# Kernel tuning notes

Hardware: AMD Instinct MI355X
Metric: run time of the kernel (lower is better)

Reference implementation:

```python
import jax, jax.numpy as jnp
import numpy as np

B, S, E, H = 2, 4096, 768, 12
D = E // H  # head_dim = 64
SCALE = D ** -0.5
NEG = -1e9


def setup_inputs() -> dict:
    key = jax.random.key(0)
    ks = jax.random.split(key, 10)
    init = lambda k, shape: jax.random.normal(k, shape, dtype=jnp.float32) * (shape[-1] ** -0.5)
    x = jax.random.normal(ks[0], (B, S, E), dtype=jnp.float32)
    attention_mask = jnp.zeros((B, 1, S, S), dtype=jnp.float32)
    # additive causal mask: 0 on/below diagonal, -1e9 above
    causal = jnp.where(jnp.tril(jnp.ones((S, S), dtype=bool)), 0.0, NEG).astype(jnp.float32)
    causal_attention_mask = causal[None, None]
    return {
        "x": x,
        "attention_mask": attention_mask,
        "causal_attention_mask": causal_attention_mask,
        "Wq": init(ks[1], (E, E)), "bq": jnp.zeros((E,), jnp.float32),
        "Wk": init(ks[2], (E, E)), "bk": jnp.zeros((E,), jnp.float32),
        "Wv": init(ks[3], (E, E)), "bv": jnp.zeros((E,), jnp.float32),
        "Wo": init(ks[4], (E, E)), "bo": jnp.zeros((E,), jnp.float32),
    }


def _split_heads(t):
    # [B,S,E] -> [B,H,S,D]
    return t.reshape(B, S, H, D).transpose(0, 2, 1, 3)


def reference(x, attention_mask, causal_attention_mask, Wq, bq, Wk, bk, Wv, bv, Wo, bo):
    q = _split_heads(x @ Wq.T + bq)
    k = _split_heads(x @ Wk.T + bk)
    v = _split_heads(x @ Wv.T + bv)
    mask = attention_mask + causal_attention_mask  # [B,1,S,S]
    scores = jnp.einsum("bhqd,bhkd->bhqk", q, k) * SCALE + mask
    probs = jax.nn.softmax(scores.astype(jnp.float32), axis=-1).astype(q.dtype)
    out = jnp.einsum("bhqk,bhkd->bhqd", probs, v)
    out = out.transpose(0, 2, 1, 3).reshape(B, S, E)
    return out @ Wo.T + bo
```

## Files before the change

kernel.cpp:

```cpp
#include <hip/hip_runtime.h>
#include <hip/hip_bf16.h>
#include <stdint.h>

#define B_ 2
#define S_ 4096
#define E_ 768
#define H_ 12
#define D_ 64
#define M_TOT (B_*S_)
#define NQKV (3*E_)

typedef __attribute__((ext_vector_type(8)))  short bf16x8;
typedef __attribute__((ext_vector_type(4)))  float f32x4;
typedef __attribute__((ext_vector_type(16))) float f32x16;
typedef unsigned short u16;
typedef unsigned int   u32;

__device__ __forceinline__ u16 f2bf(float f) {
  __hip_bfloat16 h = __float2bfloat16(f);
  return *reinterpret_cast<u16*>(&h);
}

__device__ __forceinline__ float bf2f(u16 u) {
  union { u32 i; float f; } v; v.i = ((u32)u) << 16; return v.f;
}

__device__ __forceinline__ u32 cvtpk(float lo, float hi) {
  u32 r;
  asm("v_cvt_pk_bf16_f32 %0, %1, %2" : "=v"(r) : "v"(lo), "v"(hi));
  return r;
}

#define GLDS(gp, lp) __builtin_amdgcn_global_load_lds( \
    (const __attribute__((address_space(1))) void*)(gp), \
    (__attribute__((address_space(3))) void*)(lp), 16, 0, 0)

#define QSCALE 0.1803368801111573f


__global__ void k_cast_x(const float* __restrict__ x, u16* __restrict__ xb) {
  int i = blockIdx.x * blockDim.x + threadIdx.x;
  float4 v = reinterpret_cast<const float4*>(x)[i];
  ushort4 o;
  o.x = f2bf(v.x); o.y = f2bf(v.y); o.z = f2bf(v.z); o.w = f2bf(v.w);
  reinterpret_cast<ushort4*>(xb)[i] = o;
}

__global__ void k_pack_wqkv(const float* __restrict__ Wq, const float* __restrict__ Wk,
                            const float* __restrict__ Wv, const float* __restrict__ bq,
                            const float* __restrict__ bk, const float* __restrict__ bv,
                            u16* __restrict__ wqkv, float* __restrict__ bqkv) {
  int i = blockIdx.x * blockDim.x + threadIdx.x;
  int base = i * 4;
  int n = base / E_;
  int k = base % E_;
  const float* src; float sc;
  if (n < E_)        { src = Wq + (size_t)n*E_ + k;        sc = QSCALE; }
  else if (n < 2*E_) { src = Wk + (size_t)(n-E_)*E_ + k;   sc = 1.f; }
  else               { src = Wv + (size_t)(n-2*E_)*E_ + k; sc = 1.f; }
  float4 v = *reinterpret_cast<const float4*>(src);
  ushort4 o;
  o.x = f2bf(v.x*sc); o.y = f2bf(v.y*sc); o.z = f2bf(v.z*sc); o.w = f2bf(v.w*sc);
  reinterpret_cast<ushort4*>(wqkv)[i] = o;
  if (i < NQKV) {
    float b = (i < E_) ? bq[i]*QSCALE : (i < 2*E_) ? bk[i-E_] : bv[i-2*E_];
    bqkv[i] = b;
  }
}

__global__ void k_cast_wo(const float* __restrict__ Wo, u16* __restrict__ wo) {
  int i = blockIdx.x * blockDim.x + threadIdx.x;
  float4 v = reinterpret_cast<const float4*>(Wo)[i];
  ushort4 o;
  o.x = f2bf(v.x); o.y = f2bf(v.y); o.z = f2bf(v.z); o.w = f2bf(v.w);
  reinterpret_cast<ushort4*>(wo)[i] = o;
}


template<int MODE>
__global__ __launch_bounds__(256)
void k_gemm(const u16* __restrict__ A, const u16* __restrict__ W,
            const float* __restrict__ bias,
            u16* __restrict__ dq, u16* __restrict__ dk, u16* __restrict__ dv,
            float* __restrict__ fout)
{
  constexpr int BN = (MODE == 0) ? 128 : 64;
  constexpr int NF = BN / 32;
  __shared__ u16 As[128*64];
  __shared__ u16 Ws[BN*64];
  const int tid  = threadIdx.x;
  const int lane = tid & 63, wave = tid >> 6;
  const int m0 = blockIdx.x * 128;
  const int n0 = blockIdx.y * BN;
  const int g  = lane >> 4, cc = lane & 15;
  const int wr = (wave >> 1) * 64, wc = (wave & 1) * (BN/2);
  const int srow = lane >> 3;
  const int scol = (lane & 7) * 8;

  f32x4 acc[4][NF];
  #pragma unroll
  for (int m = 0; m < 4; ++m)
    #pragma unroll
    for (int n = 0; n < NF; ++n) acc[m][n] = (f32x4){0.f,0.f,0.f,0.f};

  for (int k0 = 0; k0 < E_; k0 += 64) {
    __syncthreads();
    #pragma unroll
    for (int i = 0; i < 4; ++i) {
      const int r0 = (i*4 + wave) * 8;
      GLDS(A + (size_t)(m0 + r0 + srow)*E_ + k0 + scol, As + r0*64);
    }
    #pragma unroll
    for (int i = 0; i < BN/32; ++i) {
      const int r0 = (i*4 + wave) * 8;
      GLDS(W + (size_t)(n0 + r0 + srow)*E_ + k0 + scol, Ws + r0*64);
    }
    __syncthreads();
    #pragma unroll
    for (int kk = 0; kk < 64; kk += 32) {
      bf16x8 af[4], bfr[NF];
      #pragma unroll
      for (int m = 0; m < 4; ++m)
        af[m] = *reinterpret_cast<const bf16x8*>(As + (wr + m*16 + cc)*64 + kk + g*8);
      #pragma unroll
      for (int n = 0; n < NF; ++n)
        bfr[n] = *reinterpret_cast<const bf16x8*>(Ws + (wc + n*16 + cc)*64 + kk + g*8);
      #pragma unroll
      for (int m = 0; m < 4; ++m)
        #pragma unroll
        for (int n = 0; n < NF; ++n)
          acc[m][n] = __builtin_amdgcn_mfma_f32_16x16x32_bf16(af[m], bfr[n], acc[m][n], 0, 0, 0);
    }
  }

  #pragma unroll
  for (int n = 0; n < NF; ++n) {
    const int colg = n0 + wc + n*16 + cc;
    const float bb = bias[colg];
    if (MODE == 0) {
      const int which = colg / E_;
      const int nn = colg % E_;
      const int h = nn >> 6, d = nn & 63;
      #pragma unroll
      for (int m = 0; m < 4; ++m)
        #pragma unroll
        for (int j = 0; j < 4; ++j) {
          const int row = m0 + wr + m*16 + g*4 + j;
          const int b = row >> 12, s = row & (S_-1);
          const u16 val = f2bf(acc[m][n][j] + bb);
          if (which == 0)       dq[(((size_t)b*H_ + h)*S_ + s)*D_ + d] = val;
          else if (which == 1)  dk[(((size_t)b*H_ + h)*S_ + s)*D_ + d] = val;
          else                  dv[(((size_t)b*H_ + h)*D_ + d)*S_ + s] = val;
        }
    } else {
      #pragma unroll
      for (int m = 0; m < 4; ++m)
        #pragma unroll
        for (int j = 0; j < 4; ++j) {
          const int row = m0 + wr + m*16 + g*4 + j;
          fout[(size_t)row*E_ + colg] = acc[m][n][j] + bb;
        }
    }
  }
}


__global__ __launch_bounds__(256, 3)
void k_attn(const u16* __restrict__ Qb, const u16* __restrict__ Kb,
            const u16* __restrict__ Vtg, u16* __restrict__ AO,
            u16* __restrict__ PO, float2* __restrict__ PML)
{
  __shared__ u16 Ks[2][32*128];
  __shared__ u16 Vs[2][32*128];
  const int tid = threadIdx.x, lane = tid & 63, w = tid >> 6;

  const int L    = blockIdx.x;
  const int slot = L >> 8;
  const int cu   = L & 255;
  const int x    = cu & 7;
  const int c    = cu >> 3;
  int r;
  if (slot < 4) r = slot*32 + ((slot & 1) ? (31 - c) : c);
  else          r = 128 + c;
  int head, qt, mode;
  if (r < 120) {
    const int g_ = r / 15, o = r % 15;
    if (o < 9) {
      if (o < 3) { head = o; qt = 15 - g_; mode = 0; }
      else { const int hh = o - 3; head = hh >> 1; mode = 1 + (hh & 1); qt = 31 - 2*g_; }
    } else { const int hh = o - 9; head = hh >> 1; mode = 1 + (hh & 1); qt = 30 - 2*g_; }
  } else {
    const int rr = r - 120; qt = 7 - rr/3; head = rr % 3; mode = 0;
  }
  const int bh = x*3 + head;
  const int q0 = qt * 128;
  const int nt = (mode == 0) ? (2*qt + 2) : (qt + 1);
  const int kvtb = (mode == 2) ? (qt + 1) : 0;

  const size_t kbase = (size_t)bh * S_ * D_;
  const size_t vbase = (size_t)bh * D_ * S_;
  const int hi = lane >> 5, l31 = lane & 31;
  const int swz = (lane & 15) << 4;
  const int qg = q0 + w*32 + l31;

  int stA[2], stB[2];
  #pragma unroll
  for (int i = 0; i < 2; ++i) {
    const int jj = 2*w + i;
    const int row = jj*4 + (lane >> 4);
    const int gb = ((lane & 15) * 16) ^ ((row & 15) << 4);
    stA[i] = row + 32*(gb >> 7);
    stB[i] = (gb & 127) >> 1;
  }

  bf16x8 qf[4];
  #pragma unroll
  for (int ds = 0; ds < 4; ++ds)
    qf[ds] = *reinterpret_cast<const bf16x8*>(Qb + kbase + (size_t)qg*D_ + ds*16 + hi*8);

  float m_run = 0.f, l_run = 0.f;
  f32x16 o0, o1, cin;
  #pragma unroll
  for (int r2 = 0; r2 < 16; ++r2) { o0[r2] = 0.f; o1[r2] = 0.f; cin[r2] = 0.f; }

#define STAGE(buf, kv0_) do { \
    _Pragma("unroll") \
    for (int i = 0; i < 2; ++i) { \
      GLDS(Kb  + kbase + (size_t)((kv0_) + stA[i])*D_ + stB[i], &Ks[buf][(2*w+i)*512]); \
      GLDS(Vtg + vbase + (size_t)stA[i]*S_ + (kv0_) + stB[i],   &Vs[buf][(2*w+i)*512]); \
    } } while(0)

  int cur = 0;
  STAGE(0, kvtb*64);

  for (int it = 0; it < nt; ++it) {
    asm volatile("s_waitcnt vmcnt(0)" ::: "memory");
    __builtin_amdgcn_s_barrier();
    asm volatile("" ::: "memory");
    if (it + 1 < nt) STAGE(cur ^ 1, (kvtb + it + 1)*64);

    const int kvt = kvtb + it;
    const int kv0 = kvt * 64;
    const u16* bK = Ks[cur];
    const u16* bV = Vs[cur];

    f32x16 s0, s1;
    __builtin_amdgcn_s_setprio(1);
    {
      const int off = (16*hi ^ swz) >> 1;
      bf16x8 a0 = *reinterpret_cast<const bf16x8*>(bK + l31*128 + off);
      bf16x8 a1 = *reinterpret_cast<const bf16x8*>(bK + l31*128 + (off ^ 64));
      s0 = __builtin_amdgcn_mfma_f32_32x32x16_bf16(a0, qf[0], cin, 0, 0, 0);
      s1 = __builtin_amdgcn_mfma_f32_32x32x16_bf16(a1, qf[0], cin, 0, 0, 0);
    }
    #pragma unroll
    for (int ds = 1; ds < 4; ++ds) {
      const int off = ((32*ds + 16*hi) ^ swz) >> 1;
      bf16x8 a0 = *reinterpret_cast<const bf16x8*>(bK + l31*128 + off);
      bf16x8 a1 = *reinterpret_cast<const bf16x8*>(bK + l31*128 + (off ^ 64));
      s0 = __builtin_amdgcn_mfma_f32_32x32x16_bf16(a0, qf[ds], s0, 0, 0, 0);
      s1 = __builtin_amdgcn_mfma_f32_32x32x16_bf16(a1, qf[ds], s1, 0, 0, 0);
    }
    __builtin_amdgcn_s_setprio(0);

    if (kvt >= 2*qt) {
      #pragma unroll
      for (int r2 = 0; r2 < 16; ++r2) {
        const int kvl = kv0 + (r2&3) + 8*(r2>>2) + 4*hi;
        s0[r2] = (kvl      > qg) ? -1e30f : s0[r2];
        s1[r2] = (kvl + 32 > qg) ? -1e30f : s1[r2];
      }
    }

    #pragma unroll
    for (int r2 = 0; r2 < 16; ++r2) s0[r2] = exp2f(s0[r2]);
    #pragma unroll
    for (int r2 = 0; r2 < 16; ++r2) s1[r2] = exp2f(s1[r2]);

    float t4[8];
    #pragma unroll
    for (int i = 0; i < 4; ++i)
      t4[i] = (s0[4*i] + s0[4*i+1]) + (s0[4*i+2] + s0[4*i+3]);
    #pragma unroll
    for (int i = 0; i < 4; ++i)
      t4[4+i] = (s1[4*i] + s1[4*i+1]) + (s1[4*i+2] + s1[4*i+3]);
    float sum = ((t4[0]+t4[1]) + (t4[2]+t4[3])) + ((t4[4]+t4[5]) + (t4[6]+t4[7]));
    sum += __shfl_xor(sum, 32);

    if (__all(sum <= 1.0995116e12f)) {
      l_run += sum;
    } else {
      const float alpha = 0x1p-40f;
      l_run = (l_run + sum) * alpha;
      m_run += 40.f;
      #pragma unroll
      for (int r2 = 0; r2 < 16; ++r2) {
        s0[r2] *= alpha; s1[r2] *= alpha;
        o0[r2] *= alpha; o1[r2] *= alpha;
        cin[r2] -= 40.f;
      }
    }

    u32 c16[16];
    #pragma unroll
    for (int i = 0; i < 8; ++i) {
      c16[i]   = cvtpk(s0[2*i], s0[2*i+1]);
      c16[8+i] = cvtpk(s1[2*i], s1[2*i+1]);
    }

    #pragma unroll
    for (int ks = 0; ks < 4; ++ks) {
      const int cb = (ks>>1)*8 + (ks&1)*4;
      u32 x0 = c16[cb],   y0 = c16[cb+2];
      u32 x1 = c16[cb+1], y1 = c16[cb+3];
      asm volatile("v_permlane32_swap_b32 %0, %1" : "+v"(x0), "+v"(y0));
      asm volatile("v_permlane32_swap_b32 %0, %1" : "+v"(x1), "+v"(y1));
      union { u32 u[4]; bf16x8 v; } pf;
      pf.u[0] = x0; pf.u[1] = x1; pf.u[2] = y0; pf.u[3] = y1;
      const int voff = ((32*ks + 16*hi) ^ swz) >> 1;
      bf16x8 v0 = *reinterpret_cast<const bf16x8*>(bV + l31*128 + voff);
      bf16x8 v1 = *reinterpret_cast<const bf16x8*>(bV + l31*128 + (voff ^ 64));
      __builtin_amdgcn_s_setprio(1);
      o0 = __builtin_amdgcn_mfma_f32_32x32x16_bf16(v0, pf.v, o0, 0, 0, 0);
      o1 = __builtin_amdgcn_mfma_f32_32x32x16_bf16(v1, pf.v, o1, 0, 0, 0);
      __builtin_amdgcn_s_setprio(0);
    }

    asm volatile("" ::: "memory");
    __builtin_amdgcn_s_barrier();
    cur ^= 1;
  }
#undef STAGE

  if (mode == 0) {
    const int b = bh / H_, h = bh % H_;
    const float inv = 1.0f / l_run;
    u16* dst = AO + ((size_t)b*S_ + qg)*E_ + h*64;
    #pragma unroll
    for (int aa = 0; aa < 4; ++aa) {
      ushort4 wv;
      wv.x = f2bf(o0[4*aa+0]*inv); wv.y = f2bf(o0[4*aa+1]*inv);
      wv.z = f2bf(o0[4*aa+2]*inv); wv.w = f2bf(o0[4*aa+3]*inv);
      *reinterpret_cast<ushort4*>(dst + aa*8 + hi*4) = wv;
    }
    #pragma unroll
    for (int aa = 0; aa < 4; ++aa) {
      ushort4 wv;
      wv.x = f2bf(o1[4*aa+0]*inv); wv.y = f2bf(o1[4*aa+1]*inv);
      wv.z = f2bf(o1[4*aa+2]*inv); wv.w = f2bf(o1[4*aa+3]*inv);
      *reinterpret_cast<ushort4*>(dst + 32 + aa*8 + hi*4) = wv;
    }
  } else {
    const int qslot = (bh*16 + (qt-16))*2 + (mode - 1);
    const int rowt = w*32 + l31;
    u16* po = PO + (size_t)qslot*(128*64) + rowt*64;
    #pragma unroll
    for (int aa = 0; aa < 4; ++aa) {
      ushort4 wv;
      wv.x = f2bf(o0[4*aa+0]); wv.y = f2bf(o0[4*aa+1]);
      wv.z = f2bf(o0[4*aa+2]); wv.w = f2bf(o0[4*aa+3]);
      *reinterpret_cast<ushort4*>(po + aa*8 + hi*4) = wv;
    }
    #pragma unroll
    for (int aa = 0; aa < 4; ++aa) {
      ushort4 wv;
      wv.x = f2bf(o1[4*aa+0]); wv.y = f2bf(o1[4*aa+1]);
      wv.z = f2bf(o1[4*aa+2]); wv.w = f2bf(o1[4*aa+3]);
      *reinterpret_cast<ushort4*>(po + 32 + aa*8 + hi*4) = wv;
    }
    if (hi == 0) PML[qslot*128 + rowt] = make_float2(m_run, l_run);
  }
}


__global__ __launch_bounds__(256)
void k_comb(const u16* __restrict__ PO, const float2* __restrict__ PML,
            u16* __restrict__ AO)
{
  const int bid = blockIdx.x;
  const int bh = bid >> 4, qi = bid & 15, q = 16 + qi;
  const int t = threadIdx.x;
  const int r = t >> 1, half = t & 1;
  const int s0 = (bh*16 + qi)*2, s1 = s0 + 1;
  const float2 ml0 = PML[s0*128 + r];
  const float2 ml1 = PML[s1*128 + r];
  const float mstar = fmaxf(ml0.x, ml1.x);
  const float w0 = exp2f(ml0.x - mstar);
  const float w1 = exp2f(ml1.x - mstar);
  const float inv = 1.0f / (ml0.y*w0 + ml1.y*w1);
  const float a0 = w0 * inv, a1 = w1 * inv;
  const u16* p0 = PO + (size_t)s0*(128*64) + r*64 + half*32;
  const u16* p1 = PO + (size_t)s1*(128*64) + r*64 + half*32;
  const int b = bh / H_, h = bh % H_;
  const int row = q*128 + r;
  u16* dst = AO + ((size_t)b*S_ + row)*E_ + h*64 + half*32;
  #pragma unroll
  for (int i = 0; i < 4; ++i) {
    bf16x8 v0 = *reinterpret_cast<const bf16x8*>(p0 + i*8);
    bf16x8 v1 = *reinterpret_cast<const bf16x8*>(p1 + i*8);
    ushort4 lo, hi4;
    float f0 = bf2f(((const u16*)&v0)[0])*a0 + bf2f(((const u16*)&v1)[0])*a1;
    float f1 = bf2f(((const u16*)&v0)[1])*a0 + bf2f(((const u16*)&v1)[1])*a1;
    float f2 = bf2f(((const u16*)&v0)[2])*a0 + bf2f(((const u16*)&v1)[2])*a1;
    float f3 = bf2f(((const u16*)&v0)[3])*a0 + bf2f(((const u16*)&v1)[3])*a1;
    lo.x = f2bf(f0); lo.y = f2bf(f1); lo.z = f2bf(f2); lo.w = f2bf(f3);
    float f4 = bf2f(((const u16*)&v0)[4])*a0 + bf2f(((const u16*)&v1)[4])*a1;
    float f5 = bf2f(((const u16*)&v0)[5])*a0 + bf2f(((const u16*)&v1)[5])*a1;
    float f6 = bf2f(((const u16*)&v0)[6])*a0 + bf2f(((const u16*)&v1)[6])*a1;
    float f7 = bf2f(((const u16*)&v0)[7])*a0 + bf2f(((const u16*)&v1)[7])*a1;
    hi4.x = f2bf(f4); hi4.y = f2bf(f5); hi4.z = f2bf(f6); hi4.w = f2bf(f7);
    *reinterpret_cast<ushort4*>(dst + i*8)     = lo;
    *reinterpret_cast<ushort4*>(dst + i*8 + 4) = hi4;
  }
}


extern "C" void kernel_launch(void* const* d_in, const int* in_sizes, int n_in,
                              void* d_out, int out_size, void* d_ws, size_t ws_size,
                              hipStream_t stream) {
  const float* x  = (const float*)d_in[0];
  const float* Wq = (const float*)d_in[3];
  const float* bq = (const float*)d_in[4];
  const float* Wk = (const float*)d_in[5];
  const float* bk = (const float*)d_in[6];
  const float* Wv = (const float*)d_in[7];
  const float* bv = (const float*)d_in[8];
  const float* Wo = (const float*)d_in[9];
  const float* bo = (const float*)d_in[10];
  float* out = (float*)d_out;

  const size_t SZ_X   = (size_t)M_TOT * E_ * 2;
  const size_t SZ_WQKV= (size_t)NQKV * E_ * 2;
  const size_t SZ_WO  = (size_t)E_ * E_ * 2;
  const size_t SZ_B   = (size_t)NQKV * 4;
  char* w = (char*)d_ws;
  u16*   xb   = (u16*)(w);
  u16*   wqkv = (u16*)(w + SZ_X);
  u16*   wob  = (u16*)(w + SZ_X + SZ_WQKV);
  float* bqkv = (float*)(w + SZ_X + SZ_WQKV + SZ_WO);
  char*  w2   = w + SZ_X + SZ_WQKV + SZ_WO + SZ_B;
  u16* Qb = (u16*)(w2);
  u16* Kb = (u16*)(w2 + SZ_X);
  u16* Vb = (u16*)(w2 + 2*SZ_X);
  u16* AO = (u16*)(w2 + 3*SZ_X);
  u16* PO = xb;
  float2* PML = (float2*)(w2 + 4*SZ_X);

  k_cast_x  <<<6144, 256, 0, stream>>>(x, xb);
  k_pack_wqkv<<<1728, 256, 0, stream>>>(Wq, Wk, Wv, bq, bk, bv, wqkv, bqkv);
  k_cast_wo <<<576,  256, 0, stream>>>(Wo, wob);

  dim3 gq(64, 18);
  k_gemm<0><<<gq, 256, 0, stream>>>(xb, wqkv, bqkv, Qb, Kb, Vb, nullptr);

  k_attn<<<1152, 256, 0, stream>>>(Qb, Kb, Vb, AO, PO, PML);
  k_comb<<<384, 256, 0, stream>>>(PO, PML, AO);

  dim3 go(64, 12);
  k_gemm<1><<<go, 256, 0, stream>>>(AO, wob, bo, nullptr, nullptr, nullptr, out);
}
```

Baseline: 200.9 us.

## Split causal attention KV loop into fixed-size chunks with multi-way combine

Replaces the hand-tuned block-to-work mapping with a uniform scheme. Each query tile's causal KV range is split into chunks of 20 KV tiles, giving up to 4 chunks for late tiles, and the grid grows to one block per chunk. The first chunk writes its unnormalized partial directly into the output buffer. The combine kernel merges 2 to 4 partials per row using the saved max and sum statistics. The trailing per-iteration barrier is also dropped, since the barrier at the top of the next iteration already protects the double buffer. This aims for better load balance across CUs, at the cost of more partial-result traffic and a larger scratch footprint that spills past the reused x buffer.

```diff
diff --git a/kernel.cpp b/kernel.cpp
--- a/kernel.cpp
+++ b/kernel.cpp
@@ -174,29 +174,23 @@
   __shared__ u16 Vs[2][32*128];
   const int tid = threadIdx.x, lane = tid & 63, w = tid >> 6;
 
-  const int L    = blockIdx.x;
-  const int slot = L >> 8;
-  const int cu   = L & 255;
-  const int x    = cu & 7;
-  const int c    = cu >> 3;
-  int r;
-  if (slot < 4) r = slot*32 + ((slot & 1) ? (31 - c) : c);
-  else          r = 128 + c;
-  int head, qt, mode;
-  if (r < 120) {
-    const int g_ = r / 15, o = r % 15;
-    if (o < 9) {
-      if (o < 3) { head = o; qt = 15 - g_; mode = 0; }
-      else { const int hh = o - 3; head = hh >> 1; mode = 1 + (hh & 1); qt = 31 - 2*g_; }
-    } else { const int hh = o - 9; head = hh >> 1; mode = 1 + (hh & 1); qt = 30 - 2*g_; }
-  } else {
-    const int rr = r - 120; qt = 7 - rr/3; head = rr % 3; mode = 0;
-  }
+  const int L   = blockIdx.x;
+  const int x   = L & 7;
+  const int idx = L >> 3;
+  const int head = idx / 68;
+  const int j    = idx % 68;
+  int qt, ch;
+  if (j < 10)      { qt = j;              ch = 0; }
+  else if (j < 30) { qt = 10 + (j-10)/2;  ch = (j-10) % 2; }
+  else if (j < 60) { qt = 20 + (j-30)/3;  ch = (j-30) % 3; }
+  else             { qt = 30 + (j-60)/4;  ch = (j-60) % 4; }
   const int bh = x*3 + head;
+  const int nc = (qt + 10) / 10;
+  const int nt_full = 2*qt + 2;
+  const int kvtb = 20 * ch;
+  const int nt_c = min(nt_full, 20*(ch+1)) - kvtb;
+
   const int q0 = qt * 128;
-  const int nt = (mode == 0) ? (2*qt + 2) : (qt + 1);
-  const int kvtb = (mode == 2) ? (qt + 1) : 0;
-
   const size_t kbase = (size_t)bh * S_ * D_;
   const size_t vbase = (size_t)bh * D_ * S_;
   const int hi = lane >> 5, l31 = lane & 31;
@@ -233,11 +227,11 @@
   int cur = 0;
   STAGE(0, kvtb*64);
 
-  for (int it = 0; it < nt; ++it) {
+  for (int it = 0; it < nt_c; ++it) {
     asm volatile("s_waitcnt vmcnt(0)" ::: "memory");
     __builtin_amdgcn_s_barrier();
     asm volatile("" ::: "memory");
-    if (it + 1 < nt) STAGE(cur ^ 1, (kvtb + it + 1)*64);
+    if (it + 1 < nt_c) STAGE(cur ^ 1, (kvtb + it + 1)*64);
 
     const int kvt = kvtb + it;
     const int kv0 = kvt * 64;
@@ -326,14 +320,12 @@
       __builtin_amdgcn_s_setprio(0);
     }
 
-    asm volatile("" ::: "memory");
-    __builtin_amdgcn_s_barrier();
     cur ^= 1;
   }
 #undef STAGE
 
-  if (mode == 0) {
-    const int b = bh / H_, h = bh % H_;
+  const int b = bh / H_, h = bh % H_;
+  if (nc == 1) {
     const float inv = 1.0f / l_run;
     u16* dst = AO + ((size_t)b*S_ + qg)*E_ + h*64;
     #pragma unroll
@@ -346,14 +338,21 @@
     #pragma unroll
     for (int aa = 0; aa < 4; ++aa) {
       ushort4 wv;
+      wv.x = f2bf(o1[4*aa+0]); wv.y = f2bf(o1[4*aa+1]);
+      wv.z = f2bf(o1[4*aa+2]); wv.w = f2bf(o1[4*aa+3]);
       wv.x = f2bf(o1[4*aa+0]*inv); wv.y = f2bf(o1[4*aa+1]*inv);
       wv.z = f2bf(o1[4*aa+2]*inv); wv.w = f2bf(o1[4*aa+3]*inv);
       *reinterpret_cast<ushort4*>(dst + 32 + aa*8 + hi*4) = wv;
     }
   } else {
-    const int qslot = (bh*16 + (qt-16))*2 + (mode - 1);
+    int mbase, pbase;
+    if (qt < 20)      { mbase = (qt-10)*2;      pbase = qt-10; }
+    else if (qt < 30) { mbase = 20+(qt-20)*3;   pbase = 10+(qt-20)*2; }
+    else              { mbase = 50+(qt-30)*4;   pbase = 30+(qt-30)*3; }
     const int rowt = w*32 + l31;
-    u16* po = PO + (size_t)qslot*(128*64) + rowt*64;
+    u16* po;
+    if (ch == 0) po = AO + ((size_t)b*S_ + qg)*E_ + h*64;
+    else         po = PO + (size_t)(bh*36 + pbase + ch-1)*(128*64) + rowt*64;
     #pragma unroll
     for (int aa = 0; aa < 4; ++aa) {
       ushort4 wv;
@@ -368,7 +367,7 @@
       wv.z = f2bf(o1[4*aa+2]); wv.w = f2bf(o1[4*aa+3]);
       *reinterpret_cast<ushort4*>(po + 32 + aa*8 + hi*4) = wv;
     }
-    if (hi == 0) PML[qslot*128 + rowt] = make_float2(m_run, l_run);
+    if (hi == 0) PML[(bh*58 + mbase + ch)*128 + rowt] = make_float2(m_run, l_run);
   }
 }
 
@@ -378,37 +377,55 @@
             u16* __restrict__ AO)
 {
   const int bid = blockIdx.x;
-  const int bh = bid >> 4, qi = bid & 15, q = 16 + qi;
+  const int bh = bid / 22, qt = 10 + bid % 22;
+  const int nc = (qt + 10) / 10;
   const int t = threadIdx.x;
   const int r = t >> 1, half = t & 1;
-  const int s0 = (bh*16 + qi)*2, s1 = s0 + 1;
-  const float2 ml0 = PML[s0*128 + r];
-  const float2 ml1 = PML[s1*128 + r];
-  const float mstar = fmaxf(ml0.x, ml1.x);
-  const float w0 = exp2f(ml0.x - mstar);
-  const float w1 = exp2f(ml1.x - mstar);
-  const float inv = 1.0f / (ml0.y*w0 + ml1.y*w1);
-  const float a0 = w0 * inv, a1 = w1 * inv;
-  const u16* p0 = PO + (size_t)s0*(128*64) + r*64 + half*32;
-  const u16* p1 = PO + (size_t)s1*(128*64) + r*64 + half*32;
+  int mbase, pbase;
+  if (qt < 20)      { mbase = (qt-10)*2;      pbase = qt-10; }
+  else if (qt < 30) { mbase = 20+(qt-20)*3;   pbase = 10+(qt-20)*2; }
+  else              { mbase = 50+(qt-30)*4;   pbase = 30+(qt-30)*3; }
+  const int mslot = bh*58 + mbase;
+  const int pslot = bh*36 + pbase;
+
+  float m[4], l[4], wgt[4];
+  float mstar = -INFINITY;
+  for (int c = 0; c < nc; ++c) {
+    float2 ml = PML[(mslot + c)*128 + r];
+    m[c] = ml.x; l[c] = ml.y;
+    mstar = fmaxf(mstar, m[c]);
+  }
+  float wsum = 0.f;
+  for (int c = 0; c < nc; ++c) { wgt[c] = exp2f(m[c] - mstar); wsum += l[c]*wgt[c]; }
+  const float inv = 1.0f / wsum;
+
   const int b = bh / H_, h = bh % H_;
-  const int row = q*128 + r;
+  const int row = qt*128 + r;
   u16* dst = AO + ((size_t)b*S_ + row)*E_ + h*64 + half*32;
+
+  float acc[32];
   #pragma unroll
   for (int i = 0; i < 4; ++i) {
-    bf16x8 v0 = *reinterpret_cast<const bf16x8*>(p0 + i*8);
-    bf16x8 v1 = *reinterpret_cast<const bf16x8*>(p1 + i*8);
+    bf16x8 v = *reinterpret_cast<const bf16x8*>(dst + i*8);
+    #pragma unroll
+    for (int e = 0; e < 8; ++e) acc[i*8+e] = bf2f(((const u16*)&v)[e]) * wgt[0];
+  }
+  for (int c = 1; c < nc; ++c) {
+    const u16* p = PO + (size_t)(pslot + c-1)*(128*64) + r*64 + half*32;
+    #pragma unroll
+    for (int i = 0; i < 4; ++i) {
+      bf16x8 v = *reinterpret_cast<const bf16x8*>(p + i*8);
+      #pragma unroll
+      for (int e = 0; e < 8; ++e) acc[i*8+e] += bf2f(((const u16*)&v)[e]) * wgt[c];
+    }
+  }
+  #pragma unroll
+  for (int i = 0; i < 4; ++i) {
     ushort4 lo, hi4;
-    float f0 = bf2f(((const u16*)&v0)[0])*a0 + bf2f(((const u16*)&v1)[0])*a1;
-    float f1 = bf2f(((const u16*)&v0)[1])*a0 + bf2f(((const u16*)&v1)[1])*a1;
-    float f2 = bf2f(((const u16*)&v0)[2])*a0 + bf2f(((const u16*)&v1)[2])*a1;
-    float f3 = bf2f(((const u16*)&v0)[3])*a0 + bf2f(((const u16*)&v1)[3])*a1;
-    lo.x = f2bf(f0); lo.y = f2bf(f1); lo.z = f2bf(f2); lo.w = f2bf(f3);
-    float f4 = bf2f(((const u16*)&v0)[4])*a0 + bf2f(((const u16*)&v1)[4])*a1;
-    float f5 = bf2f(((const u16*)&v0)[5])*a0 + bf2f(((const u16*)&v1)[5])*a1;
-    float f6 = bf2f(((const u16*)&v0)[6])*a0 + bf2f(((const u16*)&v1)[6])*a1;
-    float f7 = bf2f(((const u16*)&v0)[7])*a0 + bf2f(((const u16*)&v1)[7])*a1;
-    hi4.x = f2bf(f4); hi4.y = f2bf(f5); hi4.z = f2bf(f6); hi4.w = f2bf(f7);
+    lo.x = f2bf(acc[i*8+0]*inv); lo.y = f2bf(acc[i*8+1]*inv);
+    lo.z = f2bf(acc[i*8+2]*inv); lo.w = f2bf(acc[i*8+3]*inv);
+    hi4.x = f2bf(acc[i*8+4]*inv); hi4.y = f2bf(acc[i*8+5]*inv);
+    hi4.z = f2bf(acc[i*8+6]*inv); hi4.w = f2bf(acc[i*8+7]*inv);
     *reinterpret_cast<ushort4*>(dst + i*8)     = lo;
     *reinterpret_cast<ushort4*>(dst + i*8 + 4) = hi4;
   }
@@ -453,8 +470,8 @@
   dim3 gq(64, 18);
   k_gemm<0><<<gq, 256, 0, stream>>>(xb, wqkv, bqkv, Qb, Kb, Vb, nullptr);
 
-  k_attn<<<1152, 256, 0, stream>>>(Qb, Kb, Vb, AO, PO, PML);
-  k_comb<<<384, 256, 0, stream>>>(PO, PML, AO);
+  k_attn<<<1632, 256, 0, stream>>>(Qb, Kb, Vb, AO, PO, PML);
+  k_comb<<<528, 256, 0, stream>>>(PO, PML, AO);
 
   dim3 go(64, 12);
   k_gemm<1><<<go, 256, 0, stream>>>(AO, wob, bo, nullptr, nullptr, nullptr, out);
```

Measured after the change: 215.8 us. +7.4%, slower.
